# Optimization experiments

Measured on AMD Instinct MI355X. Metric: run time of the kernel, lower is better.

The kernel has to match this reference:

```python
import jax, jax.numpy as jnp
import numpy as np

N, C = 20000, 512          # num_nodes, in_channels
E_RAND = 140000            # random edges (plus N self loops appended)
B, D = 128, 2              # num_bundles, bundle_dim
T = C // (B * D)           # feature cols per bundle (=2)
GNN_DIM = 512
NBP = B * (D * (D - 1) // 2)  # num_bun_params = 128 (1 angle per bundle since D=2)
MAX_DEG = 4
TAU = 1.0
EPS = 1e-5                 # BatchNorm1d eps


def setup_inputs() -> dict:
    key = jax.random.key(0)
    ks = jax.random.split(key, 8)
    x = jax.random.normal(ks[0], (N, C), jnp.float32)
    # edges: random + self-loops so every node has positive out-degree (finite deg_inv)
    src = jax.random.randint(ks[1], (E_RAND,), 0, N)
    dst = jax.random.randint(ks[2], (E_RAND,), 0, N)
    loop = jnp.arange(N)
    edge_index = jnp.stack([jnp.concatenate([src, loop]),
                            jnp.concatenate([dst, loop])]).astype(jnp.int64)
    s = 0.02
    W1 = jax.random.normal(ks[3], (C, GNN_DIM), jnp.float32) * s   # struct_enc lin1
    b1 = jnp.zeros((GNN_DIM,), jnp.float32)
    W2 = jax.random.normal(ks[4], (GNN_DIM, NBP), jnp.float32) * s # struct_enc lin2
    b2 = jnp.zeros((NBP,), jnp.float32)
    Wlin = jax.random.normal(ks[5], (C, C), jnp.float32) * s       # BuNNConv.lin
    blin = jnp.zeros((C,), jnp.float32)
    gamma = jnp.ones((C,), jnp.float32)                            # BatchNorm weight
    beta = jnp.zeros((C,), jnp.float32)                            # BatchNorm bias
    return dict(x=x, W1=W1, b1=b1, W2=W2, b2=b2, Wlin=Wlin, blin=blin,
                gamma=gamma, beta=beta, edge_index=edge_index)


def reference(x, W1, b1, W2, b2, Wlin, blin, gamma, beta, edge_index):
    src, dst = edge_index[0], edge_index[1]
    # degree of edge_index[0]; edge_weight = deg_inv[row] with row = edge_index[1]
    deg = jax.ops.segment_sum(jnp.ones_like(src, jnp.float32), src, num_segments=N)
    ew = (1.0 / deg)[dst]                                   # [E]

    # struct encoder (num_gnn == 0 branch): Linear -> GELU -> Linear -> 1 angle/bundle
    theta = jax.nn.gelu(x @ W1 + b1, approximate=False) @ W2 + b2   # [N, B]
    c, s = jnp.cos(theta), jnp.sin(theta)
    R = jnp.stack([jnp.stack([c, -s], -1),
                   jnp.stack([s, c], -1)], -2)              # [N, B, 2, 2] orthogonal

    # map into bundle frame
    vf = x.reshape(N, B, D, T)
    vf = jnp.einsum('nbij,nbjt->nbit', R, vf)
    h = vf.reshape(N, C)

    # truncated heat-kernel diffusion via scatter message passing
    cur = h
    for k in range(1, MAX_DEG + 1):
        agg = jax.ops.segment_sum(ew[:, None] * cur[src], dst, num_segments=N)
        cur = (-TAU / k) * (cur - agg)
        h = h + cur

    h = h @ Wlin + blin

    # map back with R^T
    vf = h.reshape(N, B, D, T)
    vf = jnp.einsum('nbji,nbjt->nbit', R, vf)
    h = vf.reshape(N, C)

    h = x + h                                # residual (dropout p = 0.0)
    mean = h.mean(axis=0)                    # BatchNorm1d, training mode, biased var
    var = h.var(axis=0)
    return (h - mean) / jnp.sqrt(var + EPS) * gamma + beta
```

## Files before the change

kernel.cpp:

```cpp
#include <hip/hip_runtime.h>

#define CC   512
#define BB_  128
#define BM 64
#define BN 128
#define BK 32

typedef __attribute__((ext_vector_type(8))) short short8;
typedef __attribute__((ext_vector_type(8))) unsigned short u16x8;
typedef __attribute__((ext_vector_type(4))) float f32x4;
typedef __attribute__((ext_vector_type(2))) float f32x2;
typedef __attribute__((ext_vector_type(4))) unsigned short u16x4;

__device__ __forceinline__ unsigned short f2bf(float f) {
  union { float f; unsigned u; } v; v.f = f;
  return (unsigned short)((v.u + 0x7FFFu + ((v.u >> 16) & 1u)) >> 16);
}
__device__ __forceinline__ float bf2f(unsigned short b) {
  union { unsigned u; float f; } v; v.u = ((unsigned)b) << 16;
  return v.f;
}

__device__ __forceinline__ void gload_lds16(const unsigned short* g, unsigned short* l) {
  __builtin_amdgcn_global_load_lds(
      (const __attribute__((address_space(1))) void*)g,
      (__attribute__((address_space(3))) void*)l, 16, 0, 0);
}

__global__ void k_zero(int* __restrict__ a, int* __restrict__ b, int* __restrict__ c,
                       float* __restrict__ d, float* __restrict__ e, int n) {
  int i = blockIdx.x * blockDim.x + threadIdx.x;
  if (i < n) { a[i] = 0; b[i] = 0; c[i] = 0; }
  if (i < CC) { d[i] = 0.f; e[i] = 0.f; }
}

__global__ void k_count(const int* __restrict__ src, const int* __restrict__ dst,
                        int* __restrict__ cnt_src, int* __restrict__ cnt_dst, int E) {
  int e = blockIdx.x * blockDim.x + threadIdx.x;
  if (e < E) {
    atomicAdd(&cnt_src[src[e]], 1);
    atomicAdd(&cnt_dst[dst[e]], 1);
  }
}

__global__ __launch_bounds__(1024) void k_scan(const int* __restrict__ cnt,
                                               int* __restrict__ rp, int n) {
  __shared__ int sm[1024];
  int tid = threadIdx.x;
  int chunk = (n + 1023) >> 10;
  int beg = tid * chunk;
  int end = beg + chunk; if (end > n) end = n;
  int s = 0;
  for (int i = beg; i < end && i < n; ++i) s += cnt[i];
  sm[tid] = s;
  __syncthreads();
  for (int off = 1; off < 1024; off <<= 1) {
    int v = (tid >= off) ? sm[tid - off] : 0;
    __syncthreads();
    sm[tid] += v;
    __syncthreads();
  }
  int run = (tid == 0) ? 0 : sm[tid - 1];
  for (int i = beg; i < end && i < n; ++i) { rp[i] = run; run += cnt[i]; }
  if (tid == 0) rp[n] = sm[1023];
}

__global__ void k_fill(const int* __restrict__ src, const int* __restrict__ dst,
                       const int* __restrict__ rp, int* __restrict__ fil,
                       int* __restrict__ col, int E) {
  int e = blockIdx.x * blockDim.x + threadIdx.x;
  if (e < E) {
    int d = dst[e];
    int p = atomicAdd(&fil[d], 1);
    col[rp[d] + p] = src[e];
  }
}

__global__ void k_conv_bf16(const float* __restrict__ in, unsigned short* __restrict__ out,
                            int validRows, int total4) {
  int i4 = blockIdx.x * blockDim.x + threadIdx.x;
  if (i4 >= total4) return;
  int row = i4 / (CC / 4);
  u16x4 o;
  if (row < validRows) {
    f32x4 v = ((const f32x4*)in)[i4];
    o[0] = f2bf(v[0]); o[1] = f2bf(v[1]); o[2] = f2bf(v[2]); o[3] = f2bf(v[3]);
  } else {
    o[0] = 0; o[1] = 0; o[2] = 0; o[3] = 0;
  }
  ((u16x4*)out)[i4] = o;
}

__global__ void k_transconv_all(const float* __restrict__ W1, const float* __restrict__ W2,
                                const float* __restrict__ Wlin,
                                unsigned short* __restrict__ W1t, unsigned short* __restrict__ W2t,
                                unsigned short* __restrict__ Wlt) {
  const float* W; unsigned short* Wt; int K, Nw;
  if (blockIdx.z == 0)      { W = W1;   Wt = W1t; K = 512; Nw = 512; }
  else if (blockIdx.z == 1) { W = W2;   Wt = W2t; K = 512; Nw = 128; if (blockIdx.x >= 4) return; }
  else                      { W = Wlin; Wt = Wlt; K = 512; Nw = 512; }
  __shared__ float tile[32][33];
  int n0 = blockIdx.x * 32, k0 = blockIdx.y * 32;
  int tx = threadIdx.x, ty = threadIdx.y;
  for (int j = 0; j < 4; ++j)
    tile[ty + j * 8][tx] = W[(k0 + ty + j * 8) * Nw + n0 + tx];
  __syncthreads();
  for (int j = 0; j < 4; ++j)
    Wt[(n0 + ty + j * 8) * K + k0 + tx] = f2bf(tile[tx][ty + j * 8]);
}

template <int EPI>
__device__ __forceinline__ void epi_store(float v, int row, int colL, void* outp,
                                          const float* x, unsigned short* c0,
                                          int Nw, int nvalid) {
  if (EPI == 0) {
    ((float*)outp)[(size_t)row * Nw + colL] = v;
  } else if (EPI == 1) {
    float g = 0.5f * v * (1.0f + erff(v * 0.70710678118654752f));
    ((unsigned short*)outp)[(size_t)row * Nw + colL] = f2bf(g);
  } else {
    size_t bidx = (size_t)row * Nw + colL;
    if (row < nvalid) {
      float sv, cv;
      sincosf(v, &sv, &cv);
      f32x2 o; o[0] = cv; o[1] = sv;
      ((f32x2*)outp)[bidx] = o;
      f32x4 xv = ((const f32x4*)x)[bidx];
      u16x4 rr;
      rr[0] = f2bf(cv * xv[0] - sv * xv[2]);
      rr[1] = f2bf(cv * xv[1] - sv * xv[3]);
      rr[2] = f2bf(sv * xv[0] + cv * xv[2]);
      rr[3] = f2bf(sv * xv[1] + cv * xv[3]);
      ((u16x4*)c0)[bidx] = rr;
    } else {
      u16x4 rr; rr[0] = 0; rr[1] = 0; rr[2] = 0; rr[3] = 0;
      ((u16x4*)c0)[bidx] = rr;
    }
  }
}

template <int EPI>
__global__ __launch_bounds__(256) void k_gemm(const unsigned short* __restrict__ A,
                                              const unsigned short* __restrict__ Bt,
                                              const float* __restrict__ bias,
                                              void* __restrict__ outp,
                                              const float* __restrict__ x,
                                              unsigned short* __restrict__ c0,
                                              const f32x2* __restrict__ csr,
                                              float* __restrict__ csum,
                                              float* __restrict__ csq,
                                              int K, int Nw, int nvalid) {
  __shared__ unsigned short As[2][BM * BK];
  __shared__ unsigned short Bs[2][BN * BK];
  __shared__ float s_sum[BN], s_sq[BN];
  const int m0 = blockIdx.x * BM;
  const int n0 = blockIdx.y * BN;
  const int tid = threadIdx.x;
  const int wid = tid >> 6, lane = tid & 63;
  const int wr = wid >> 1, wc = wid & 1;
  const int l15 = lane & 15, kg = lane >> 4;
  const int arow = wid * 16 + (lane >> 2);
  const int aseg = (lane & 3) * 8;

  if (EPI == 3 && tid < BN) { s_sum[tid] = 0.f; s_sq[tid] = 0.f; }

  f32x4 acc00 = {}, acc01 = {}, acc02 = {}, acc03 = {};
  f32x4 acc10 = {}, acc11 = {}, acc12 = {}, acc13 = {};

  const int nt = K / BK;
  gload_lds16(&A[(size_t)(m0 + arow) * K + aseg],       &As[0][wid * 512]);
  gload_lds16(&Bt[(size_t)(n0 + arow) * K + aseg],      &Bs[0][wid * 512]);
  gload_lds16(&Bt[(size_t)(n0 + 64 + arow) * K + aseg], &Bs[0][2048 + wid * 512]);
  __syncthreads();

  for (int kk = 0; kk < nt; ++kk) {
    const int cur = kk & 1;
    if (kk + 1 < nt) {
      const int kt = (kk + 1) * BK;
      gload_lds16(&A[(size_t)(m0 + arow) * K + kt + aseg],       &As[cur ^ 1][wid * 512]);
      gload_lds16(&Bt[(size_t)(n0 + arow) * K + kt + aseg],      &Bs[cur ^ 1][wid * 512]);
      gload_lds16(&Bt[(size_t)(n0 + 64 + arow) * K + kt + aseg], &Bs[cur ^ 1][2048 + wid * 512]);
    }
    short8 af0 = *(const short8*)&As[cur][(wr * 32 +  0 + l15) * BK + kg * 8];
    short8 af1 = *(const short8*)&As[cur][(wr * 32 + 16 + l15) * BK + kg * 8];
    short8 bg0 = *(const short8*)&Bs[cur][(wc * 64 +  0 + l15) * BK + kg * 8];
    short8 bg1 = *(const short8*)&Bs[cur][(wc * 64 + 16 + l15) * BK + kg * 8];
    short8 bg2 = *(const short8*)&Bs[cur][(wc * 64 + 32 + l15) * BK + kg * 8];
    short8 bg3 = *(const short8*)&Bs[cur][(wc * 64 + 48 + l15) * BK + kg * 8];
    acc00 = __builtin_amdgcn_mfma_f32_16x16x32_bf16(af0, bg0, acc00, 0, 0, 0);
    acc01 = __builtin_amdgcn_mfma_f32_16x16x32_bf16(af0, bg1, acc01, 0, 0, 0);
    acc02 = __builtin_amdgcn_mfma_f32_16x16x32_bf16(af0, bg2, acc02, 0, 0, 0);
    acc03 = __builtin_amdgcn_mfma_f32_16x16x32_bf16(af0, bg3, acc03, 0, 0, 0);
    acc10 = __builtin_amdgcn_mfma_f32_16x16x32_bf16(af1, bg0, acc10, 0, 0, 0);
    acc11 = __builtin_amdgcn_mfma_f32_16x16x32_bf16(af1, bg1, acc11, 0, 0, 0);
    acc12 = __builtin_amdgcn_mfma_f32_16x16x32_bf16(af1, bg2, acc12, 0, 0, 0);
    acc13 = __builtin_amdgcn_mfma_f32_16x16x32_bf16(af1, bg3, acc13, 0, 0, 0);
    __syncthreads();
  }

  if (EPI != 3) {
#define DO_EPI(ACC, MI, NI)                                                     \
  do {                                                                          \
    const int row_ = m0 + wr * 32 + (MI) * 16 + kg * 4;                         \
    const int col_ = n0 + wc * 64 + (NI) * 16 + l15;                            \
    const float b_ = bias[col_];                                                \
    epi_store<EPI>(ACC[0] + b_, row_ + 0, col_, outp, x, c0, Nw, nvalid);       \
    epi_store<EPI>(ACC[1] + b_, row_ + 1, col_, outp, x, c0, Nw, nvalid);       \
    epi_store<EPI>(ACC[2] + b_, row_ + 2, col_, outp, x, c0, Nw, nvalid);       \
    epi_store<EPI>(ACC[3] + b_, row_ + 3, col_, outp, x, c0, Nw, nvalid);       \
  } while (0)

    DO_EPI(acc00, 0, 0); DO_EPI(acc01, 0, 1); DO_EPI(acc02, 0, 2); DO_EPI(acc03, 0, 3);
    DO_EPI(acc10, 1, 0); DO_EPI(acc11, 1, 1); DO_EPI(acc12, 1, 2); DO_EPI(acc13, 1, 3);
#undef DO_EPI
  } else {
    float pS0 = 0.f, pS1 = 0.f, pS2 = 0.f, pS3 = 0.f;
    float pQ0 = 0.f, pQ1 = 0.f, pQ2 = 0.f, pQ3 = 0.f;
    const int bi = (l15 >> 1) & 1;
#define DO_EPI3(ACC, MI, NI, PS, PQ)                                            \
  do {                                                                          \
    const int row_ = m0 + wr * 32 + (MI) * 16 + kg * 4;                         \
    const int col_ = n0 + wc * 64 + (NI) * 16 + l15;                            \
    const float b_ = bias[col_];                                                \
    _Pragma("unroll")                                                           \
    for (int r = 0; r < 4; ++r) {                                               \
      float v = ACC[r] + b_;                                                    \
      float vp = __shfl_xor(v, 2);           \
      int rr_ = row_ + r;                                                       \
      if (rr_ < nvalid) {                                                       \
        f32x2 a = csr[(size_t)rr_ * BB_ + (col_ >> 2)];                         \
        float ov = bi == 0 ? a[0] * v + a[1] * vp : a[0] * v - a[1] * vp;       \
        ov += x[(size_t)rr_ * CC + col_];                                       \
        ((float*)outp)[(size_t)rr_ * CC + col_] = ov;                           \
        PS += ov; PQ += ov * ov;                                                \
      }                                                                         \
    }                                                                           \
  } while (0)

    DO_EPI3(acc00, 0, 0, pS0, pQ0); DO_EPI3(acc01, 0, 1, pS1, pQ1);
    DO_EPI3(acc02, 0, 2, pS2, pQ2); DO_EPI3(acc03, 0, 3, pS3, pQ3);
    DO_EPI3(acc10, 1, 0, pS0, pQ0); DO_EPI3(acc11, 1, 1, pS1, pQ1);
    DO_EPI3(acc12, 1, 2, pS2, pQ2); DO_EPI3(acc13, 1, 3, pS3, pQ3);
#undef DO_EPI3
    const int cb = wc * 64 + l15;
    atomicAdd(&s_sum[cb +  0], pS0); atomicAdd(&s_sq[cb +  0], pQ0);
    atomicAdd(&s_sum[cb + 16], pS1); atomicAdd(&s_sq[cb + 16], pQ1);
    atomicAdd(&s_sum[cb + 32], pS2); atomicAdd(&s_sq[cb + 32], pQ2);
    atomicAdd(&s_sum[cb + 48], pS3); atomicAdd(&s_sq[cb + 48], pQ3);
    __syncthreads();
    if (tid < BN) {
      atomicAdd(&csum[n0 + tid], s_sum[tid]);
      atomicAdd(&csq[n0 + tid], s_sq[tid]);
    }
  }
}

__global__ __launch_bounds__(256) void k_diffuse(const unsigned short* __restrict__ cur,
                                                 unsigned short* __restrict__ nxt,
                                                 const int* __restrict__ cnt_src,
                                                 const int* __restrict__ rp,
                                                 const int* __restrict__ col,
                                                 float coef, int n) {
  int w = threadIdx.x >> 6, lane = threadIdx.x & 63;
  int v = blockIdx.x * 4 + w;
  if (v >= n) return;
  int beg = rp[v], end = rp[v + 1];
  const u16x8* curv = (const u16x8*)cur;
  float s[8] = {0.f,0.f,0.f,0.f,0.f,0.f,0.f,0.f};
  for (int e = beg; e < end; ++e) {
    int u = col[e];
    u16x8 r = curv[(size_t)u * 64 + lane];
    #pragma unroll
    for (int j = 0; j < 8; ++j) s[j] += bf2f(r[j]);
  }
  float di = 1.0f / (float)cnt_src[v];
  u16x8 cv = curv[(size_t)v * 64 + lane];
  u16x8 o;
  #pragma unroll
  for (int j = 0; j < 8; ++j) o[j] = f2bf((bf2f(cv[j]) - s[j] * di) * coef);
  ((u16x8*)nxt)[(size_t)v * 64 + lane] = o;
}

__global__ __launch_bounds__(256) void k_diffuse_final(const unsigned short* __restrict__ c0,
                                                       const unsigned short* __restrict__ c1,
                                                       const unsigned short* __restrict__ c2,
                                                       const unsigned short* __restrict__ cur,
                                                       unsigned short* __restrict__ hb,
                                                       const int* __restrict__ cnt_src,
                                                       const int* __restrict__ rp,
                                                       const int* __restrict__ col,
                                                       float coef, int n) {
  int w = threadIdx.x >> 6, lane = threadIdx.x & 63;
  int v = blockIdx.x * 4 + w;
  if (v >= n) return;
  int beg = rp[v], end = rp[v + 1];
  const u16x8* curv = (const u16x8*)cur;
  float s[8] = {0.f,0.f,0.f,0.f,0.f,0.f,0.f,0.f};
  for (int e = beg; e < end; ++e) {
    int u = col[e];
    u16x8 r = curv[(size_t)u * 64 + lane];
    #pragma unroll
    for (int j = 0; j < 8; ++j) s[j] += bf2f(r[j]);
  }
  float di = 1.0f / (float)cnt_src[v];
  size_t o = (size_t)v * 64 + lane;
  u16x8 cv = curv[o];
  u16x8 a0 = ((const u16x8*)c0)[o];
  u16x8 a1 = ((const u16x8*)c1)[o];
  u16x8 a2 = ((const u16x8*)c2)[o];
  u16x8 hv;
  #pragma unroll
  for (int j = 0; j < 8; ++j) {
    float c3v = bf2f(cv[j]);
    float c4v = (c3v - s[j] * di) * coef;
    hv[j] = f2bf(bf2f(a0[j]) + bf2f(a1[j]) + bf2f(a2[j]) + c3v + c4v);
  }
  ((u16x8*)hb)[o] = hv;
}

__global__ __launch_bounds__(256) void k_norm(float* __restrict__ out,
                                              const float* __restrict__ colsum,
                                              const float* __restrict__ colsq,
                                              const float* __restrict__ gamma,
                                              const float* __restrict__ beta,
                                              float invn, int n4) {
  __shared__ float ssc[CC], ssh[CC];
  int t = threadIdx.x;
  for (int c = t; c < CC; c += 256) {
    float mean = colsum[c] * invn;
    float var = colsq[c] * invn - mean * mean;
    float sc = gamma[c] * rsqrtf(var + 1e-5f);
    ssc[c] = sc;
    ssh[c] = beta[c] - mean * sc;
  }
  __syncthreads();
  int i = blockIdx.x * blockDim.x + t;
  if (i >= n4) return;
  int c4 = i & (CC / 4 - 1);
  f32x4 v = ((f32x4*)out)[i];
  f32x4 sc = *(const f32x4*)&ssc[c4 * 4];
  f32x4 sh = *(const f32x4*)&ssh[c4 * 4];
  ((f32x4*)out)[i] = v * sc + sh;
}

extern "C" void kernel_launch(void* const* d_in, const int* in_sizes, int n_in,
                              void* d_out, int out_size, void* d_ws, size_t ws_size,
                              hipStream_t stream) {
  (void)n_in; (void)out_size; (void)ws_size;
  const float* x    = (const float*)d_in[0];
  const float* W1   = (const float*)d_in[1];
  const float* b1   = (const float*)d_in[2];
  const float* W2   = (const float*)d_in[3];
  const float* b2   = (const float*)d_in[4];
  const float* Wlin = (const float*)d_in[5];
  const float* blin = (const float*)d_in[6];
  const float* gamma = (const float*)d_in[7];
  const float* beta  = (const float*)d_in[8];
  const int*   ei    = (const int*)d_in[9];

  const int n   = in_sizes[0] / CC;
  const int E   = in_sizes[9] / 2;
  const int GNN = in_sizes[2];
  const int NBP = in_sizes[4];
  const int* src = ei;
  const int* dst = ei + E;
  const int mt64 = (n + BM - 1) / BM;
  const int mpad = 20096;
  const size_t SB = (size_t)mpad * CC;

  char* ws = (char*)d_ws;
  size_t off = 0;
  auto alloc = [&](size_t bytes) -> void* {
    void* p = ws + off;
    off = (off + bytes + 255) & ~(size_t)255;
    return p;
  };
  int*   cnt_src = (int*)alloc((size_t)n * 4);
  int*   cnt_dst = (int*)alloc((size_t)n * 4);
  int*   fil     = (int*)alloc((size_t)n * 4);
  int*   rp      = (int*)alloc((size_t)(n + 1) * 4);
  int*   colx    = (int*)alloc((size_t)E * 4);
  float* colsum  = (float*)alloc(CC * 4);
  float* colsq   = (float*)alloc(CC * 4);
  unsigned short* W1t = (unsigned short*)alloc((size_t)GNN * CC * 2);
  unsigned short* W2t = (unsigned short*)alloc((size_t)NBP * GNN * 2);
  unsigned short* Wlt = (unsigned short*)alloc((size_t)CC * CC * 2);
  f32x2* cs = (f32x2*)alloc((size_t)mpad * BB_ * 8);
  unsigned short* c0 = (unsigned short*)alloc(SB * 2);
  unsigned short* c1 = (unsigned short*)alloc(SB * 2);
  unsigned short* c2 = (unsigned short*)alloc(SB * 2);
  unsigned short* c3 = (unsigned short*)alloc(SB * 2);
  unsigned short* hb = (unsigned short*)alloc(SB * 2);
  unsigned short* xb = c0;
  unsigned short* G  = c1;

  k_zero<<<(n + 255) / 256, 256, 0, stream>>>(cnt_src, cnt_dst, fil, colsum, colsq, n);

  k_count<<<(E + 255) / 256, 256, 0, stream>>>(src, dst, cnt_src, cnt_dst, E);
  k_scan<<<1, 1024, 0, stream>>>(cnt_dst, rp, n);
  k_fill<<<(E + 255) / 256, 256, 0, stream>>>(src, dst, rp, fil, colx, E);

  int total4 = mpad * (CC / 4);
  k_conv_bf16<<<(total4 + 255) / 256, 256, 0, stream>>>(x, xb, n, total4);
  k_transconv_all<<<dim3(16, 16, 3), dim3(32, 8), 0, stream>>>(W1, W2, Wlin, W1t, W2t, Wlt);

  k_gemm<1><<<dim3(mt64, GNN / BN), 256, 0, stream>>>(xb, W1t, b1, (void*)G, nullptr, nullptr,
                                                      nullptr, nullptr, nullptr, CC, GNN, n);
  k_gemm<2><<<dim3(mt64, NBP / BN), 256, 0, stream>>>(G, W2t, b2, (void*)cs, x, c0,
                                                      nullptr, nullptr, nullptr, GNN, NBP, n);

  k_diffuse<<<(n + 3) / 4, 256, 0, stream>>>(c0, c1, cnt_src, rp, colx, -1.0f, n);
  k_diffuse<<<(n + 3) / 4, 256, 0, stream>>>(c1, c2, cnt_src, rp, colx, -0.5f, n);
  k_diffuse<<<(n + 3) / 4, 256, 0, stream>>>(c2, c3, cnt_src, rp, colx, -(1.0f / 3.0f), n);
  k_diffuse_final<<<(n + 3) / 4, 256, 0, stream>>>(c0, c1, c2, c3, hb, cnt_src, rp, colx, -0.25f, n);

  k_gemm<3><<<dim3(mt64, CC / BN), 256, 0, stream>>>(hb, Wlt, blin, d_out, x, nullptr,
                                                     cs, colsum, colsq, CC, CC, n);

  int nb = n * BB_;
  k_norm<<<(nb + 255) / 256, 256, 0, stream>>>((float*)d_out, colsum, colsq, gamma, beta,
                                               1.0f / (float)n, nb);
}
```

Before: 319.7 us.

## Pre-pack GEMM operands into MFMA fragment layout and load directly from global

```diff
diff --git a/kernel.cpp b/kernel.cpp
--- a/kernel.cpp
+++ b/kernel.cpp
@@ -4,7 +4,6 @@
 #define BB_  128
 #define BM 64
 #define BN 128
-#define BK 32
 
 typedef __attribute__((ext_vector_type(8))) short short8;
 typedef __attribute__((ext_vector_type(8))) unsigned short u16x8;
@@ -21,10 +20,9 @@
   return v.f;
 }
 
-__device__ __forceinline__ void gload_lds16(const unsigned short* g, unsigned short* l) {
-  __builtin_amdgcn_global_load_lds(
-      (const __attribute__((address_space(1))) void*)g,
-      (__attribute__((address_space(3))) void*)l, 16, 0, 0);
+__device__ __forceinline__ size_t pidx(int row, int k, int K32) {
+  return ((size_t)((row >> 4) * K32 + (k >> 5)) << 9) +
+         (size_t)(((row & 15) + ((k >> 3) & 3) * 16) << 3) + (k & 7);
 }
 
 __global__ void k_zero(int* __restrict__ a, int* __restrict__ b, int* __restrict__ c,
@@ -76,29 +74,33 @@
   }
 }
 
-__global__ void k_conv_bf16(const float* __restrict__ in, unsigned short* __restrict__ out,
-                            int validRows, int total4) {
-  int i4 = blockIdx.x * blockDim.x + threadIdx.x;
-  if (i4 >= total4) return;
-  int row = i4 / (CC / 4);
-  u16x4 o;
+__global__ void k_conv_pan(const float* __restrict__ in, unsigned short* __restrict__ out,
+                           int validRows, int total8) {
+  int i = blockIdx.x * blockDim.x + threadIdx.x;
+  if (i >= total8) return;
+  int row = i >> 6;
+  int c = (i & 63) << 3;
+  u16x8 o;
   if (row < validRows) {
-    f32x4 v = ((const f32x4*)in)[i4];
-    o[0] = f2bf(v[0]); o[1] = f2bf(v[1]); o[2] = f2bf(v[2]); o[3] = f2bf(v[3]);
+    f32x4 v0 = ((const f32x4*)in)[(i << 1)];
+    f32x4 v1 = ((const f32x4*)in)[(i << 1) + 1];
+    o[0] = f2bf(v0[0]); o[1] = f2bf(v0[1]); o[2] = f2bf(v0[2]); o[3] = f2bf(v0[3]);
+    o[4] = f2bf(v1[0]); o[5] = f2bf(v1[1]); o[6] = f2bf(v1[2]); o[7] = f2bf(v1[3]);
   } else {
-    o[0] = 0; o[1] = 0; o[2] = 0; o[3] = 0;
-  }
-  ((u16x4*)out)[i4] = o;
+    #pragma unroll
+    for (int j = 0; j < 8; ++j) o[j] = 0;
+  }
+  *(u16x8*)&out[pidx(row, c, CC >> 5)] = o;
 }
 
 __global__ void k_transconv_all(const float* __restrict__ W1, const float* __restrict__ W2,
                                 const float* __restrict__ Wlin,
                                 unsigned short* __restrict__ W1t, unsigned short* __restrict__ W2t,
                                 unsigned short* __restrict__ Wlt) {
-  const float* W; unsigned short* Wt; int K, Nw;
-  if (blockIdx.z == 0)      { W = W1;   Wt = W1t; K = 512; Nw = 512; }
-  else if (blockIdx.z == 1) { W = W2;   Wt = W2t; K = 512; Nw = 128; if (blockIdx.x >= 4) return; }
-  else                      { W = Wlin; Wt = Wlt; K = 512; Nw = 512; }
+  const float* W; unsigned short* Wt; int Nw;
+  if (blockIdx.z == 0)      { W = W1;   Wt = W1t; Nw = 512; }
+  else if (blockIdx.z == 1) { W = W2;   Wt = W2t; Nw = 128; if (blockIdx.x >= 4) return; }
+  else                      { W = Wlin; Wt = Wlt; Nw = 512; }
   __shared__ float tile[32][33];
   int n0 = blockIdx.x * 32, k0 = blockIdx.y * 32;
   int tx = threadIdx.x, ty = threadIdx.y;
@@ -106,7 +108,7 @@
     tile[ty + j * 8][tx] = W[(k0 + ty + j * 8) * Nw + n0 + tx];
   __syncthreads();
   for (int j = 0; j < 4; ++j)
-    Wt[(n0 + ty + j * 8) * K + k0 + tx] = f2bf(tile[tx][ty + j * 8]);
+    Wt[pidx(n0 + ty + j * 8, k0 + tx, 16)] = f2bf(tile[tx][ty + j * 8]);
 }
 
 template <int EPI>
@@ -117,7 +119,7 @@
     ((float*)outp)[(size_t)row * Nw + colL] = v;
   } else if (EPI == 1) {
     float g = 0.5f * v * (1.0f + erff(v * 0.70710678118654752f));
-    ((unsigned short*)outp)[(size_t)row * Nw + colL] = f2bf(g);
+    ((unsigned short*)outp)[pidx(row, colL, Nw >> 5)] = f2bf(g);
   } else {
     size_t bidx = (size_t)row * Nw + colL;
     if (row < nvalid) {
@@ -150,8 +152,6 @@
                                               float* __restrict__ csum,
                                               float* __restrict__ csq,
                                               int K, int Nw, int nvalid) {
-  __shared__ unsigned short As[2][BM * BK];
-  __shared__ unsigned short Bs[2][BN * BK];
   __shared__ float s_sum[BN], s_sq[BN];
   const int m0 = blockIdx.x * BM;
   const int n0 = blockIdx.y * BN;
@@ -159,34 +159,32 @@
   const int wid = tid >> 6, lane = tid & 63;
   const int wr = wid >> 1, wc = wid & 1;
   const int l15 = lane & 15, kg = lane >> 4;
-  const int arow = wid * 16 + (lane >> 2);
-  const int aseg = (lane & 3) * 8;
-
-  if (EPI == 3 && tid < BN) { s_sum[tid] = 0.f; s_sq[tid] = 0.f; }
+  const int K32 = K >> 5;
+
+  if (EPI == 3) {
+    if (tid < BN) { s_sum[tid] = 0.f; s_sq[tid] = 0.f; }
+    __syncthreads();
+  }
+
+  const unsigned short* pa0 = A + (((size_t)((m0 >> 4) + wr * 2 + 0) * K32) << 9) + lane * 8;
+  const unsigned short* pa1 = A + (((size_t)((m0 >> 4) + wr * 2 + 1) * K32) << 9) + lane * 8;
+  const unsigned short* pb0 = Bt + (((size_t)((n0 >> 4) + wc * 4 + 0) * K32) << 9) + lane * 8;
+  const unsigned short* pb1 = Bt + (((size_t)((n0 >> 4) + wc * 4 + 1) * K32) << 9) + lane * 8;
+  const unsigned short* pb2 = Bt + (((size_t)((n0 >> 4) + wc * 4 + 2) * K32) << 9) + lane * 8;
+  const unsigned short* pb3 = Bt + (((size_t)((n0 >> 4) + wc * 4 + 3) * K32) << 9) + lane * 8;
 
   f32x4 acc00 = {}, acc01 = {}, acc02 = {}, acc03 = {};
   f32x4 acc10 = {}, acc11 = {}, acc12 = {}, acc13 = {};
 
-  const int nt = K / BK;
-  gload_lds16(&A[(size_t)(m0 + arow) * K + aseg],       &As[0][wid * 512]);
-  gload_lds16(&Bt[(size_t)(n0 + arow) * K + aseg],      &Bs[0][wid * 512]);
-  gload_lds16(&Bt[(size_t)(n0 + 64 + arow) * K + aseg], &Bs[0][2048 + wid * 512]);
-  __syncthreads();
-
-  for (int kk = 0; kk < nt; ++kk) {
-    const int cur = kk & 1;
-    if (kk + 1 < nt) {
-      const int kt = (kk + 1) * BK;
-      gload_lds16(&A[(size_t)(m0 + arow) * K + kt + aseg],       &As[cur ^ 1][wid * 512]);
-      gload_lds16(&Bt[(size_t)(n0 + arow) * K + kt + aseg],      &Bs[cur ^ 1][wid * 512]);
-      gload_lds16(&Bt[(size_t)(n0 + 64 + arow) * K + kt + aseg], &Bs[cur ^ 1][2048 + wid * 512]);
-    }
-    short8 af0 = *(const short8*)&As[cur][(wr * 32 +  0 + l15) * BK + kg * 8];
-    short8 af1 = *(const short8*)&As[cur][(wr * 32 + 16 + l15) * BK + kg * 8];
-    short8 bg0 = *(const short8*)&Bs[cur][(wc * 64 +  0 + l15) * BK + kg * 8];
-    short8 bg1 = *(const short8*)&Bs[cur][(wc * 64 + 16 + l15) * BK + kg * 8];
-    short8 bg2 = *(const short8*)&Bs[cur][(wc * 64 + 32 + l15) * BK + kg * 8];
-    short8 bg3 = *(const short8*)&Bs[cur][(wc * 64 + 48 + l15) * BK + kg * 8];
+  #pragma unroll 4
+  for (int kt = 0; kt < K32; ++kt) {
+    const size_t o = (size_t)kt << 9;
+    short8 af0 = *(const short8*)(pa0 + o);
+    short8 af1 = *(const short8*)(pa1 + o);
+    short8 bg0 = *(const short8*)(pb0 + o);
+    short8 bg1 = *(const short8*)(pb1 + o);
+    short8 bg2 = *(const short8*)(pb2 + o);
+    short8 bg3 = *(const short8*)(pb3 + o);
     acc00 = __builtin_amdgcn_mfma_f32_16x16x32_bf16(af0, bg0, acc00, 0, 0, 0);
     acc01 = __builtin_amdgcn_mfma_f32_16x16x32_bf16(af0, bg1, acc01, 0, 0, 0);
     acc02 = __builtin_amdgcn_mfma_f32_16x16x32_bf16(af0, bg2, acc02, 0, 0, 0);
@@ -195,7 +193,6 @@
     acc11 = __builtin_amdgcn_mfma_f32_16x16x32_bf16(af1, bg1, acc11, 0, 0, 0);
     acc12 = __builtin_amdgcn_mfma_f32_16x16x32_bf16(af1, bg2, acc12, 0, 0, 0);
     acc13 = __builtin_amdgcn_mfma_f32_16x16x32_bf16(af1, bg3, acc13, 0, 0, 0);
-    __syncthreads();
   }
 
   if (EPI != 3) {
@@ -315,7 +312,7 @@
     float c4v = (c3v - s[j] * di) * coef;
     hv[j] = f2bf(bf2f(a0[j]) + bf2f(a1[j]) + bf2f(a2[j]) + c3v + c4v);
   }
-  ((u16x8*)hb)[o] = hv;
+  *(u16x8*)&hb[pidx(v, lane << 3, CC >> 5)] = hv;
 }
 
 __global__ __launch_bounds__(256) void k_norm(float* __restrict__ out,
@@ -391,8 +388,8 @@
   unsigned short* c2 = (unsigned short*)alloc(SB * 2);
   unsigned short* c3 = (unsigned short*)alloc(SB * 2);
   unsigned short* hb = (unsigned short*)alloc(SB * 2);
-  unsigned short* xb = c0;
-  unsigned short* G  = c1;
+  unsigned short* xb = (unsigned short*)alloc(SB * 2);
+  unsigned short* G  = (unsigned short*)alloc(SB * 2);
 
   k_zero<<<(n + 255) / 256, 256, 0, stream>>>(cnt_src, cnt_dst, fil, colsum, colsq, n);
 
@@ -400,8 +397,8 @@
   k_scan<<<1, 1024, 0, stream>>>(cnt_dst, rp, n);
   k_fill<<<(E + 255) / 256, 256, 0, stream>>>(src, dst, rp, fil, colx, E);
 
-  int total4 = mpad * (CC / 4);
-  k_conv_bf16<<<(total4 + 255) / 256, 256, 0, stream>>>(x, xb, n, total4);
+  int total8 = mpad * (CC / 8);
+  k_conv_pan<<<(total8 + 255) / 256, 256, 0, stream>>>(x, xb, n, total8);
   k_transconv_all<<<dim3(16, 16, 3), dim3(32, 8), 0, stream>>>(W1, W2, Wlin, W1t, W2t, Wlt);
 
   k_gemm<1><<<dim3(mt64, GNN / BN), 256, 0, stream>>>(xb, W1t, b1, (void*)G, nullptr, nullptr,
```

Measured after the change: 323.9 us. Within noise of the previous version (+1.3%).

## Triple-buffer GEMM LDS tiles with explicit vmcnt waits and barriers

Applied to the files above, without the earlier changes.

```diff
diff --git a/kernel.cpp b/kernel.cpp
--- a/kernel.cpp
+++ b/kernel.cpp
@@ -150,8 +150,8 @@
                                               float* __restrict__ csum,
                                               float* __restrict__ csq,
                                               int K, int Nw, int nvalid) {
-  __shared__ unsigned short As[2][BM * BK];
-  __shared__ unsigned short Bs[2][BN * BK];
+  __shared__ unsigned short As[3][BM * BK];
+  __shared__ unsigned short Bs[3][BN * BK];
   __shared__ float s_sum[BN], s_sq[BN];
   const int m0 = blockIdx.x * BM;
   const int n0 = blockIdx.y * BN;
@@ -162,31 +162,36 @@
   const int arow = wid * 16 + (lane >> 2);
   const int aseg = (lane & 3) * 8;
 
-  if (EPI == 3 && tid < BN) { s_sum[tid] = 0.f; s_sq[tid] = 0.f; }
+  if (EPI == 3) {
+    if (tid < BN) { s_sum[tid] = 0.f; s_sq[tid] = 0.f; }
+    __syncthreads();
+  }
 
   f32x4 acc00 = {}, acc01 = {}, acc02 = {}, acc03 = {};
   f32x4 acc10 = {}, acc11 = {}, acc12 = {}, acc13 = {};
 
   const int nt = K / BK;
-  gload_lds16(&A[(size_t)(m0 + arow) * K + aseg],       &As[0][wid * 512]);
-  gload_lds16(&Bt[(size_t)(n0 + arow) * K + aseg],      &Bs[0][wid * 512]);
-  gload_lds16(&Bt[(size_t)(n0 + 64 + arow) * K + aseg], &Bs[0][2048 + wid * 512]);
-  __syncthreads();
+  #pragma unroll
+  for (int t = 0; t < 3; ++t) {
+    const int kt = t * BK;
+    gload_lds16(&A[(size_t)(m0 + arow) * K + kt + aseg],       &As[t][wid * 512]);
+    gload_lds16(&Bt[(size_t)(n0 + arow) * K + kt + aseg],      &Bs[t][wid * 512]);
+    gload_lds16(&Bt[(size_t)(n0 + 64 + arow) * K + kt + aseg], &Bs[t][2048 + wid * 512]);
+  }
 
   for (int kk = 0; kk < nt; ++kk) {
-    const int cur = kk & 1;
-    if (kk + 1 < nt) {
-      const int kt = (kk + 1) * BK;
-      gload_lds16(&A[(size_t)(m0 + arow) * K + kt + aseg],       &As[cur ^ 1][wid * 512]);
-      gload_lds16(&Bt[(size_t)(n0 + arow) * K + kt + aseg],      &Bs[cur ^ 1][wid * 512]);
-      gload_lds16(&Bt[(size_t)(n0 + 64 + arow) * K + kt + aseg], &Bs[cur ^ 1][2048 + wid * 512]);
-    }
-    short8 af0 = *(const short8*)&As[cur][(wr * 32 +  0 + l15) * BK + kg * 8];
-    short8 af1 = *(const short8*)&As[cur][(wr * 32 + 16 + l15) * BK + kg * 8];
-    short8 bg0 = *(const short8*)&Bs[cur][(wc * 64 +  0 + l15) * BK + kg * 8];
-    short8 bg1 = *(const short8*)&Bs[cur][(wc * 64 + 16 + l15) * BK + kg * 8];
-    short8 bg2 = *(const short8*)&Bs[cur][(wc * 64 + 32 + l15) * BK + kg * 8];
-    short8 bg3 = *(const short8*)&Bs[cur][(wc * 64 + 48 + l15) * BK + kg * 8];
+    const int buf = kk % 3;
+    if (kk < nt - 2)       asm volatile("s_waitcnt vmcnt(6)" ::: "memory");
+    else if (kk == nt - 2) asm volatile("s_waitcnt vmcnt(3)" ::: "memory");
+    else                   asm volatile("s_waitcnt vmcnt(0)" ::: "memory");
+    __builtin_amdgcn_s_barrier();
+    __builtin_amdgcn_sched_barrier(0);
+    short8 af0 = *(const short8*)&As[buf][(wr * 32 +  0 + l15) * BK + kg * 8];
+    short8 af1 = *(const short8*)&As[buf][(wr * 32 + 16 + l15) * BK + kg * 8];
+    short8 bg0 = *(const short8*)&Bs[buf][(wc * 64 +  0 + l15) * BK + kg * 8];
+    short8 bg1 = *(const short8*)&Bs[buf][(wc * 64 + 16 + l15) * BK + kg * 8];
+    short8 bg2 = *(const short8*)&Bs[buf][(wc * 64 + 32 + l15) * BK + kg * 8];
+    short8 bg3 = *(const short8*)&Bs[buf][(wc * 64 + 48 + l15) * BK + kg * 8];
     acc00 = __builtin_amdgcn_mfma_f32_16x16x32_bf16(af0, bg0, acc00, 0, 0, 0);
     acc01 = __builtin_amdgcn_mfma_f32_16x16x32_bf16(af0, bg1, acc01, 0, 0, 0);
     acc02 = __builtin_amdgcn_mfma_f32_16x16x32_bf16(af0, bg2, acc02, 0, 0, 0);
@@ -195,7 +200,14 @@
     acc11 = __builtin_amdgcn_mfma_f32_16x16x32_bf16(af1, bg1, acc11, 0, 0, 0);
     acc12 = __builtin_amdgcn_mfma_f32_16x16x32_bf16(af1, bg2, acc12, 0, 0, 0);
     acc13 = __builtin_amdgcn_mfma_f32_16x16x32_bf16(af1, bg3, acc13, 0, 0, 0);
-    __syncthreads();
+    __builtin_amdgcn_sched_barrier(0);
+    __builtin_amdgcn_s_barrier();
+    if (kk + 3 < nt) {
+      const int kt = (kk + 3) * BK;
+      gload_lds16(&A[(size_t)(m0 + arow) * K + kt + aseg],       &As[buf][wid * 512]);
+      gload_lds16(&Bt[(size_t)(n0 + arow) * K + kt + aseg],      &Bs[buf][wid * 512]);
+      gload_lds16(&Bt[(size_t)(n0 + 64 + arow) * K + kt + aseg], &Bs[buf][2048 + wid * 512]);
+    }
   }
 
   if (EPI != 3) {
```

After: 342.3 us. +7.1%, slower.
